# Kernel optimization log

Measured on AMD Instinct MI355X. Metric: run time of the kernel, lower is better.

Reference implementation:

```python
import math
import jax, jax.numpy as jnp
import numpy as np

K = 4            # ensemble size
S_CONST = 0.25   # isotropic gaussian scale constant
GAUSS_DIM = 6

def pixel_shuffle(x, r):
    B, C, H, W = x.shape
    C2 = C // (r * r)
    x = x.reshape(B, C2, r, r, H, W).transpose(0, 1, 4, 2, 5, 3)
    return x.reshape(B, C2, H * r, W * r)

def pixel_unshuffle(x, r):
    B, C, H, W = x.shape
    x = x.reshape(B, C, H // r, r, W // r, r).transpose(0, 1, 3, 5, 2, 4)
    return x.reshape(B, C * r * r, H // r, W // r)

def setup_inputs():
    key = jax.random.key(0)
    k1, k2, k3 = jax.random.split(key, 3)
    B, h, w = 4, 128, 128
    inp = jax.random.normal(k1, (B, 3, h, w), jnp.float32)
    w_enc = jax.random.normal(k2, (1024, 3, 3, 3), jnp.float32) * 0.05
    b_enc = jnp.zeros((1024,), jnp.float32)
    w_head = jax.random.normal(k3, (GAUSS_DIM * K, 256), jnp.float32) * 0.05
    b_head = jnp.zeros((GAUSS_DIM * K,), jnp.float32)
    return {"inp": inp, "w_enc": w_enc, "b_enc": b_enc,
            "w_head": w_head, "b_head": b_head, "scale": 2}

def _forward(inp, w_enc, b_enc, w_head, b_head, scale):
    B, _, h, w = inp.shape
    s1 = s2 = float(scale)
    H, W = round(h * s1), round(w * s2)
    # --- encoder (conv3x3 -> pixel_shuffle x4 -> 64ch @ 4h x 4w) ---
    x = jax.lax.conv_general_dilated(inp, w_enc, (1, 1), 'SAME',
        dimension_numbers=('NCHW', 'OIHW', 'NCHW')) + b_enc[None, :, None, None]
    x = pixel_shuffle(x, 4)                 # [B, 64, 4h, 4w]
    feat = pixel_unshuffle(x, 2)            # [B, 256, 2h, 2w]
    # --- gauss head (1x1 conv) ---
    pred_map = jnp.einsum('bchw,oc->bohw', feat, w_head) + b_head[None, :, None, None]
    gh, gw = 2 * h, 2 * w
    N = gh * gw
    pred = pred_map.reshape(B, GAUSS_DIM * K, N).transpose(0, 2, 1).reshape(B, N, K, GAUSS_DIM)
    rgb_k, off_raw, w_logits = pred[..., :3], pred[..., 3:5], pred[..., 5:6]
    wgt = jax.nn.softmax(w_logits, axis=2)
    rgb = (rgb_k * wgt).sum(2)              # [B, N, 3]
    off = (jnp.tanh(off_raw) * wgt).sum(2)  # [B, N, 2]
    # --- gaussian centers in NDC ---
    yi, xi = jnp.meshgrid(jnp.arange(gh), jnp.arange(gw), indexing='ij')
    coordx = (xi / gw * 2.0 - 1.0).reshape(-1).astype(jnp.float32)
    coordy = (yi / gh * 2.0 - 1.0).reshape(-1).astype(jnp.float32)
    x_ndc = coordx[None, :] + 2.0 * off[..., 0] / w - 1.0 / W
    y_ndc = coordy[None, :] + 2.0 * off[..., 1] / h - 1.0 / H
    # --- rasterize: isotropic gaussians, local 3-sigma window, scatter-add ---
    s_px = S_CONST * s1                     # pixel-space std (theta = 0)
    r = max(2, int(math.ceil(3.0 * s_px)))
    offs = jnp.arange(-r, r + 1)

    def raster_one(xn, yn, col):
        cx = 0.5 * ((xn + 1.0) * W - 1.0)   # ndc -> pixel center
        cy = 0.5 * ((yn + 1.0) * H - 1.0)
        px = jnp.floor(cx)[:, None] + offs  # [N, 2r+1]
        py = jnp.floor(cy)[:, None] + offs
        dx = px - cx[:, None]
        dy = py - cy[:, None]
        power = -0.5 * (dy[:, :, None] ** 2 + dx[:, None, :] ** 2) / (s_px * s_px)
        alpha = jnp.minimum(0.999, jnp.exp(power))
        alpha = jnp.where(alpha > 1.0 / 255.0, alpha, 0.0)   # kernel alpha cutoff
        pxi = px.astype(jnp.int32)
        pyi = py.astype(jnp.int32)
        valid = ((pyi[:, :, None] >= 0) & (pyi[:, :, None] < H) &
                 (pxi[:, None, :] >= 0) & (pxi[:, None, :] < W))
        contrib = jnp.where(valid, alpha, 0.0)               # [N, wy, wx]
        yfull = jnp.clip(jnp.broadcast_to(pyi[:, :, None], contrib.shape), 0, H - 1)
        xfull = jnp.clip(jnp.broadcast_to(pxi[:, None, :], contrib.shape), 0, W - 1)
        img = jnp.zeros((H, W, 3), jnp.float32).at[yfull, xfull].add(
            contrib[..., None] * col[:, None, None, :])
        return jnp.clip(img, 0.0, 1.0).transpose(2, 0, 1)    # [3, H, W]

    return jax.vmap(raster_one)(x_ndc, y_ndc, rgb)

def reference(inp, w_enc, b_enc, w_head, b_head, scale):
    return _forward(inp, w_enc, b_enc, w_head, b_head, scale)
```

## Files before the change

kernel.cpp:

```cpp
#include <hip/hip_runtime.h>
#include <math.h>

#define NB 4
#define IH 128
#define IW 128
#define GH 256
#define GW 256
#define NGAUSS (NB * GH * GW)

#define WEFF_FLOATS (4 * 24 * 27)
#define BEFF_FLOATS (4 * 24)
#define POS_OFF 2688
#define CR_OFF (POS_OFF + 2 * NGAUSS)
#define CG_OFF (CR_OFF + NGAUSS)
#define CB_OFF (CG_OFF + NGAUSS)

#define TSX 16
#define TSY 16
#define GR 24
#define NREG (GR * GR)
#define RR_MAX 2.770360f
#define EXP2C (-2.8853900818f)

__device__ __forceinline__ float fast_tanh(float x) {
  return 1.f - 2.f / (__expf(2.f * x) + 1.f);
}
__device__ __forceinline__ float clamp01(float v) {
  return fminf(1.f, fmaxf(0.f, v));
}

__global__ __launch_bounds__(256) void weff_kernel(
    const float* __restrict__ w_enc, const float* __restrict__ b_enc,
    const float* __restrict__ w_head, const float* __restrict__ b_head,
    float* __restrict__ weff, float* __restrict__ beff) {
  __shared__ float sWH[24 * 256];
  __shared__ float sWE[256 * 27];
  __shared__ float sBE[256];

  int tid = (int)threadIdx.x;
  int p = (int)blockIdx.x;
  int ph = p >> 1, pw = p & 1;

  for (int i = tid; i < 24 * 256; i += 256) sWH[i] = w_head[i];
  {
    int hc = tid;
    int ch = ((hc >> 2) << 4) + (2 * ph + ((hc >> 1) & 1)) * 4 + (2 * pw + (hc & 1));
    for (int t = 0; t < 27; ++t) sWE[hc * 27 + t] = w_enc[ch * 27 + t];
    sBE[hc] = b_enc[ch];
  }
  __syncthreads();

  for (int j = tid; j < 24 * 27; j += 256) {
    int o = j / 27, t = j % 27;
    float a = 0.f;
    for (int hc = 0; hc < 256; ++hc) a = fmaf(sWH[o * 256 + hc], sWE[hc * 27 + t], a);
    weff[p * (24 * 27) + j] = a;
  }
  if (tid < 24) {
    float a = b_head[tid];
    for (int hc = 0; hc < 256; ++hc) a = fmaf(sWH[tid * 256 + hc], sBE[hc], a);
    beff[p * 24 + tid] = a;
  }
}

__global__ __launch_bounds__(256) void gauss_kernel(
    const float* __restrict__ inp, const float* __restrict__ ws_ro,
    float* __restrict__ ws) {
  __shared__ float sW[4 * 24 * 28];
  __shared__ float sB[BEFF_FLOATS];

  int tid = (int)threadIdx.x;
  for (int i = tid; i < 4 * 24 * 28; i += 256) {
    int row = i / 28, k = i - row * 28;
    sW[i] = (k < 27) ? ws_ro[row * 27 + k] : 0.f;
  }
  for (int i = tid; i < BEFF_FLOATS; i += 256) sB[i] = ws_ro[WEFF_FLOATS + i];
  __syncthreads();

  int bid = (int)blockIdx.x;
  int b = bid >> 7;
  int t = bid & 127;
  int TYg = (t >> 3) * 16;
  int TXg = (t & 7) * 32;
  int hh = TYg + (tid >> 4);
  int ww0 = TXg + (tid & 15);
  int p = (hh & 1) * 2 + (ww0 & 1);
  int hs = hh >> 1, ws0 = ww0 >> 1;

  const float* ib = inp + b * 3 * IH * IW;
  float in0[28], in1[28];
  in0[27] = 0.f; in1[27] = 0.f;
  #pragma unroll
  for (int cin = 0; cin < 3; ++cin) {
    #pragma unroll
    for (int ky = 0; ky < 3; ++ky) {
      int y = hs + ky - 1;
      bool yok = (y >= 0 && y < IH);
      #pragma unroll
      for (int kx = 0; kx < 3; ++kx) {
        int x0 = ws0 + kx - 1;
        int x1 = x0 + 8;
        float v0 = 0.f, v1 = 0.f;
        if (yok && x0 >= 0 && x0 < IW) v0 = ib[(cin * IH + y) * IW + x0];
        if (yok && x1 < IW) v1 = ib[(cin * IH + y) * IW + x1];
        in0[cin * 9 + ky * 3 + kx] = v0;
        in1[cin * 9 + ky * 3 + kx] = v1;
      }
    }
  }

  float a0[24], a1[24];
  #pragma unroll
  for (int o = 0; o < 24; ++o) { float bi = sB[p * 24 + o]; a0[o] = bi; a1[o] = bi; }
  #pragma unroll
  for (int o = 0; o < 24; ++o) {
    const float4* wrow = (const float4*)&sW[(p * 24 + o) * 28];
    #pragma unroll
    for (int kq = 0; kq < 7; ++kq) {
      float4 w = wrow[kq];
      a0[o] = fmaf(in0[kq * 4 + 0], w.x, a0[o]);
      a0[o] = fmaf(in0[kq * 4 + 1], w.y, a0[o]);
      a0[o] = fmaf(in0[kq * 4 + 2], w.z, a0[o]);
      a0[o] = fmaf(in0[kq * 4 + 3], w.w, a0[o]);
      a1[o] = fmaf(in1[kq * 4 + 0], w.x, a1[o]);
      a1[o] = fmaf(in1[kq * 4 + 1], w.y, a1[o]);
      a1[o] = fmaf(in1[kq * 4 + 2], w.z, a1[o]);
      a1[o] = fmaf(in1[kq * 4 + 3], w.w, a1[o]);
    }
  }

  float2* posP = (float2*)(ws + POS_OFF);

  #pragma unroll
  for (int which = 0; which < 2; ++which) {
    const float* pr = which ? a1 : a0;
    int ww = which ? (ww0 + 16) : ww0;

    float l0 = pr[5], l1 = pr[11], l2 = pr[17], l3 = pr[23];
    float m = fmaxf(fmaxf(l0, l1), fmaxf(l2, l3));
    float e0 = __expf(l0 - m), e1 = __expf(l1 - m);
    float e2 = __expf(l2 - m), e3 = __expf(l3 - m);
    float inv = 1.f / (e0 + e1 + e2 + e3);
    float w0 = e0 * inv, w1 = e1 * inv, w2 = e2 * inv, w3 = e3 * inv;
    float cr = w0 * pr[0] + w1 * pr[6] + w2 * pr[12] + w3 * pr[18];
    float cg = w0 * pr[1] + w1 * pr[7] + w2 * pr[13] + w3 * pr[19];
    float cb = w0 * pr[2] + w1 * pr[8] + w2 * pr[14] + w3 * pr[20];
    float ox = w0 * fast_tanh(pr[3]) + w1 * fast_tanh(pr[9]) +
               w2 * fast_tanh(pr[15]) + w3 * fast_tanh(pr[21]);
    float oy = w0 * fast_tanh(pr[4]) + w1 * fast_tanh(pr[10]) +
               w2 * fast_tanh(pr[16]) + w3 * fast_tanh(pr[22]);

    float coordx = ((float)ww / 256.f) * 2.f - 1.f;
    float coordy = ((float)hh / 256.f) * 2.f - 1.f;
    float x_ndc = coordx + 2.f * ox / 128.f - 1.f / 256.f;
    float y_ndc = coordy + 2.f * oy / 128.f - 1.f / 256.f;
    float cx = 0.5f * ((x_ndc + 1.f) * 256.f - 1.f);
    float cy = 0.5f * ((y_ndc + 1.f) * 256.f - 1.f);

    int g = (b << 16) | (hh << 8) | ww;
    posP[g] = make_float2(cy, cx);
    ws[CR_OFF + g] = cr;
    ws[CG_OFF + g] = cg;
    ws[CB_OFF + g] = cb;
  }
}

__global__ __launch_bounds__(256) void gather_kernel(
    const float* __restrict__ ws, float* __restrict__ out) {
  __shared__ float2 sPos[NREG];
  __shared__ float4 sCol[NREG];

  int tid = (int)threadIdx.x;
  int bid = (int)blockIdx.x;
  int b = bid >> 8;
  int t = bid & 255;
  int TY = (t >> 4) * TSY;
  int TX = (t & 15) * TSX;
  const float2* posP = (const float2*)(ws + POS_OFF);

  for (int i = tid; i < NREG; i += 256) {
    int r = i / GR, c = i - r * GR;
    int hh = TY - 3 + r, ww = TX - 3 + c;
    if ((unsigned)hh < GH && (unsigned)ww < GW) {
      int g = (b << 16) | (hh << 8) | ww;
      sPos[i] = posP[g];
      sCol[i] = make_float4(ws[CR_OFF + g], ws[CG_OFF + g], ws[CB_OFF + g], 0.f);
    } else {
      sPos[i] = make_float2(1e9f, 1e9f);
      sCol[i] = make_float4(0.f, 0.f, 0.f, 0.f);
    }
  }
  __syncthreads();

  int pxl = tid & 15, pyl = tid >> 4;
  float fpx = (float)(TX + pxl), fpy = (float)(TY + pyl);
  float ar = 0.f, ag = 0.f, ab = 0.f;

  #pragma unroll
  for (int ry = 0; ry < 8; ++ry) {
    int base = (pyl + ry) * GR + pxl;
    #pragma unroll
    for (int rx = 0; rx < 8; ++rx) {
      float2 P = sPos[base + rx];
      float dy = fpy - P.x;
      float dx = fpx - P.y;
      float rr = fmaf(dy, dy, dx * dx);
      if (rr < RR_MAX) {
        float al = fminf(0.999f, exp2f(EXP2C * rr));
        float4 C = sCol[base + rx];
        ar = fmaf(al, C.x, ar);
        ag = fmaf(al, C.y, ag);
        ab = fmaf(al, C.z, ab);
      }
    }
  }

  float* ob = out + b * 3 * GH * GW;
  int i0 = (TY + pyl) * GW + (TX + pxl);
  ob[i0] = clamp01(ar);
  ob[GH * GW + i0] = clamp01(ag);
  ob[2 * GH * GW + i0] = clamp01(ab);
}

extern "C" void kernel_launch(void* const* d_in, const int* in_sizes, int n_in,
                              void* d_out, int out_size, void* d_ws, size_t ws_size,
                              hipStream_t stream) {
  const float* inp = (const float*)d_in[0];
  const float* w_enc = (const float*)d_in[1];
  const float* b_enc = (const float*)d_in[2];
  const float* w_head = (const float*)d_in[3];
  const float* b_head = (const float*)d_in[4];

  float* ws = (float*)d_ws;
  float* weff = ws;
  float* beff = ws + WEFF_FLOATS;

  weff_kernel<<<4, 256, 0, stream>>>(w_enc, b_enc, w_head, b_head, weff, beff);

  gauss_kernel<<<512, 256, 0, stream>>>(inp, ws, ws);

  gather_kernel<<<NB * 256, 256, 0, stream>>>(ws, (float*)d_out);
}
```

Measured before the change: 100.8 us.

## Pack gaussian colors as float4, shrink gather halo, one gaussian per thread

Colors are now stored as one interleaved float4 per gaussian instead of three planar arrays, so the gather stage loads them with a single vector load. The gather neighborhood shrinks from an 8x8 window (24x24 region) to 7x7 (22x22 region) on the assumption that offsets stay within two cells. Each gauss_kernel thread now computes one gaussian instead of two, with twice as many blocks and occupancy hints in launch_bounds on both kernels. The smaller window could drop contributions if a gaussian center drifts further than the new halo covers.

```diff
diff --git a/kernel.cpp b/kernel.cpp
--- a/kernel.cpp
+++ b/kernel.cpp
@@ -11,13 +11,11 @@
 #define WEFF_FLOATS (4 * 24 * 27)
 #define BEFF_FLOATS (4 * 24)
 #define POS_OFF 2688
-#define CR_OFF (POS_OFF + 2 * NGAUSS)
-#define CG_OFF (CR_OFF + NGAUSS)
-#define CB_OFF (CG_OFF + NGAUSS)
+#define COL_OFF (POS_OFF + 2 * NGAUSS)
 
 #define TSX 16
 #define TSY 16
-#define GR 24
+#define GR 22
 #define NREG (GR * GR)
 #define RR_MAX 2.770360f
 #define EXP2C (-2.8853900818f)
@@ -63,7 +61,7 @@
   }
 }
 
-__global__ __launch_bounds__(256) void gauss_kernel(
+__global__ __launch_bounds__(256, 4) void gauss_kernel(
     const float* __restrict__ inp, const float* __restrict__ ws_ro,
     float* __restrict__ ws) {
   __shared__ float sW[4 * 24 * 28];
@@ -78,18 +76,16 @@
   __syncthreads();
 
   int bid = (int)blockIdx.x;
-  int b = bid >> 7;
-  int t = bid & 127;
-  int TYg = (t >> 3) * 16;
-  int TXg = (t & 7) * 32;
-  int hh = TYg + (tid >> 4);
-  int ww0 = TXg + (tid & 15);
-  int p = (hh & 1) * 2 + (ww0 & 1);
-  int hs = hh >> 1, ws0 = ww0 >> 1;
+  int b = bid >> 8;
+  int t = bid & 255;
+  int hh = (t >> 4) * 16 + (tid >> 4);
+  int ww = (t & 15) * 16 + (tid & 15);
+  int p = (hh & 1) * 2 + (ww & 1);
+  int hs = hh >> 1, ws_ = ww >> 1;
 
   const float* ib = inp + b * 3 * IH * IW;
-  float in0[28], in1[28];
-  in0[27] = 0.f; in1[27] = 0.f;
+  float in[28];
+  in[27] = 0.f;
   #pragma unroll
   for (int cin = 0; cin < 3; ++cin) {
     #pragma unroll
@@ -98,74 +94,57 @@
       bool yok = (y >= 0 && y < IH);
       #pragma unroll
       for (int kx = 0; kx < 3; ++kx) {
-        int x0 = ws0 + kx - 1;
-        int x1 = x0 + 8;
-        float v0 = 0.f, v1 = 0.f;
-        if (yok && x0 >= 0 && x0 < IW) v0 = ib[(cin * IH + y) * IW + x0];
-        if (yok && x1 < IW) v1 = ib[(cin * IH + y) * IW + x1];
-        in0[cin * 9 + ky * 3 + kx] = v0;
-        in1[cin * 9 + ky * 3 + kx] = v1;
+        int x = ws_ + kx - 1;
+        float v = 0.f;
+        if (yok && x >= 0 && x < IW) v = ib[(cin * IH + y) * IW + x];
+        in[cin * 9 + ky * 3 + kx] = v;
       }
     }
   }
 
-  float a0[24], a1[24];
-  #pragma unroll
-  for (int o = 0; o < 24; ++o) { float bi = sB[p * 24 + o]; a0[o] = bi; a1[o] = bi; }
+  float pr[24];
   #pragma unroll
   for (int o = 0; o < 24; ++o) {
+    float a = sB[p * 24 + o];
     const float4* wrow = (const float4*)&sW[(p * 24 + o) * 28];
     #pragma unroll
     for (int kq = 0; kq < 7; ++kq) {
       float4 w = wrow[kq];
-      a0[o] = fmaf(in0[kq * 4 + 0], w.x, a0[o]);
-      a0[o] = fmaf(in0[kq * 4 + 1], w.y, a0[o]);
-      a0[o] = fmaf(in0[kq * 4 + 2], w.z, a0[o]);
-      a0[o] = fmaf(in0[kq * 4 + 3], w.w, a0[o]);
-      a1[o] = fmaf(in1[kq * 4 + 0], w.x, a1[o]);
-      a1[o] = fmaf(in1[kq * 4 + 1], w.y, a1[o]);
-      a1[o] = fmaf(in1[kq * 4 + 2], w.z, a1[o]);
-      a1[o] = fmaf(in1[kq * 4 + 3], w.w, a1[o]);
-    }
-  }
-
-  float2* posP = (float2*)(ws + POS_OFF);
-
-  #pragma unroll
-  for (int which = 0; which < 2; ++which) {
-    const float* pr = which ? a1 : a0;
-    int ww = which ? (ww0 + 16) : ww0;
-
-    float l0 = pr[5], l1 = pr[11], l2 = pr[17], l3 = pr[23];
-    float m = fmaxf(fmaxf(l0, l1), fmaxf(l2, l3));
-    float e0 = __expf(l0 - m), e1 = __expf(l1 - m);
-    float e2 = __expf(l2 - m), e3 = __expf(l3 - m);
-    float inv = 1.f / (e0 + e1 + e2 + e3);
-    float w0 = e0 * inv, w1 = e1 * inv, w2 = e2 * inv, w3 = e3 * inv;
-    float cr = w0 * pr[0] + w1 * pr[6] + w2 * pr[12] + w3 * pr[18];
-    float cg = w0 * pr[1] + w1 * pr[7] + w2 * pr[13] + w3 * pr[19];
-    float cb = w0 * pr[2] + w1 * pr[8] + w2 * pr[14] + w3 * pr[20];
-    float ox = w0 * fast_tanh(pr[3]) + w1 * fast_tanh(pr[9]) +
-               w2 * fast_tanh(pr[15]) + w3 * fast_tanh(pr[21]);
-    float oy = w0 * fast_tanh(pr[4]) + w1 * fast_tanh(pr[10]) +
-               w2 * fast_tanh(pr[16]) + w3 * fast_tanh(pr[22]);
-
-    float coordx = ((float)ww / 256.f) * 2.f - 1.f;
-    float coordy = ((float)hh / 256.f) * 2.f - 1.f;
-    float x_ndc = coordx + 2.f * ox / 128.f - 1.f / 256.f;
-    float y_ndc = coordy + 2.f * oy / 128.f - 1.f / 256.f;
-    float cx = 0.5f * ((x_ndc + 1.f) * 256.f - 1.f);
-    float cy = 0.5f * ((y_ndc + 1.f) * 256.f - 1.f);
-
-    int g = (b << 16) | (hh << 8) | ww;
-    posP[g] = make_float2(cy, cx);
-    ws[CR_OFF + g] = cr;
-    ws[CG_OFF + g] = cg;
-    ws[CB_OFF + g] = cb;
-  }
-}
-
-__global__ __launch_bounds__(256) void gather_kernel(
+      a = fmaf(in[kq * 4 + 0], w.x, a);
+      a = fmaf(in[kq * 4 + 1], w.y, a);
+      a = fmaf(in[kq * 4 + 2], w.z, a);
+      a = fmaf(in[kq * 4 + 3], w.w, a);
+    }
+    pr[o] = a;
+  }
+
+  float l0 = pr[5], l1 = pr[11], l2 = pr[17], l3 = pr[23];
+  float m = fmaxf(fmaxf(l0, l1), fmaxf(l2, l3));
+  float e0 = __expf(l0 - m), e1 = __expf(l1 - m);
+  float e2 = __expf(l2 - m), e3 = __expf(l3 - m);
+  float inv = 1.f / (e0 + e1 + e2 + e3);
+  float w0 = e0 * inv, w1 = e1 * inv, w2 = e2 * inv, w3 = e3 * inv;
+  float cr = w0 * pr[0] + w1 * pr[6] + w2 * pr[12] + w3 * pr[18];
+  float cg = w0 * pr[1] + w1 * pr[7] + w2 * pr[13] + w3 * pr[19];
+  float cb = w0 * pr[2] + w1 * pr[8] + w2 * pr[14] + w3 * pr[20];
+  float ox = w0 * fast_tanh(pr[3]) + w1 * fast_tanh(pr[9]) +
+             w2 * fast_tanh(pr[15]) + w3 * fast_tanh(pr[21]);
+  float oy = w0 * fast_tanh(pr[4]) + w1 * fast_tanh(pr[10]) +
+             w2 * fast_tanh(pr[16]) + w3 * fast_tanh(pr[22]);
+
+  float coordx = ((float)ww / 256.f) * 2.f - 1.f;
+  float coordy = ((float)hh / 256.f) * 2.f - 1.f;
+  float x_ndc = coordx + 2.f * ox / 128.f - 1.f / 256.f;
+  float y_ndc = coordy + 2.f * oy / 128.f - 1.f / 256.f;
+  float cx = 0.5f * ((x_ndc + 1.f) * 256.f - 1.f);
+  float cy = 0.5f * ((y_ndc + 1.f) * 256.f - 1.f);
+
+  int g = (b << 16) | (hh << 8) | ww;
+  ((float2*)(ws + POS_OFF))[g] = make_float2(cy, cx);
+  ((float4*)(ws + COL_OFF))[g] = make_float4(cr, cg, cb, 0.f);
+}
+
+__global__ __launch_bounds__(256, 4) void gather_kernel(
     const float* __restrict__ ws, float* __restrict__ out) {
   __shared__ float2 sPos[NREG];
   __shared__ float4 sCol[NREG];
@@ -177,14 +156,15 @@
   int TY = (t >> 4) * TSY;
   int TX = (t & 15) * TSX;
   const float2* posP = (const float2*)(ws + POS_OFF);
+  const float4* colP = (const float4*)(ws + COL_OFF);
 
   for (int i = tid; i < NREG; i += 256) {
     int r = i / GR, c = i - r * GR;
-    int hh = TY - 3 + r, ww = TX - 3 + c;
+    int hh = TY - 2 + r, ww = TX - 2 + c;
     if ((unsigned)hh < GH && (unsigned)ww < GW) {
       int g = (b << 16) | (hh << 8) | ww;
       sPos[i] = posP[g];
-      sCol[i] = make_float4(ws[CR_OFF + g], ws[CG_OFF + g], ws[CB_OFF + g], 0.f);
+      sCol[i] = colP[g];
     } else {
       sPos[i] = make_float2(1e9f, 1e9f);
       sCol[i] = make_float4(0.f, 0.f, 0.f, 0.f);
@@ -197,10 +177,10 @@
   float ar = 0.f, ag = 0.f, ab = 0.f;
 
   #pragma unroll
-  for (int ry = 0; ry < 8; ++ry) {
+  for (int ry = 0; ry < 7; ++ry) {
     int base = (pyl + ry) * GR + pxl;
     #pragma unroll
-    for (int rx = 0; rx < 8; ++rx) {
+    for (int rx = 0; rx < 7; ++rx) {
       float2 P = sPos[base + rx];
       float dy = fpy - P.x;
       float dx = fpx - P.y;
@@ -237,7 +217,7 @@
 
   weff_kernel<<<4, 256, 0, stream>>>(w_enc, b_enc, w_head, b_head, weff, beff);
 
-  gauss_kernel<<<512, 256, 0, stream>>>(inp, ws, ws);
+  gauss_kernel<<<NB * 256, 256, 0, stream>>>(inp, ws, ws);
 
   gather_kernel<<<NB * 256, 256, 0, stream>>>(ws, (float*)d_out);
 }
```

Measured after the change: 112.9 us. +12.0%, slower.
